# Kernel tuning notes

Measured on AMD Instinct MI355X. Metric: run time of the kernel, lower is better.

The kernel has to match this reference:

```python
import jax, jax.numpy as jnp
import numpy as np

B, TQ, TK = 4, 128, 512
DQ = DK = DV = H = 1024


def setup_inputs() -> dict:
    key = jax.random.key(0)
    ks = jax.random.split(key, 7)
    s = 0.05  # keep tanh out of saturation
    return {
        "query": jax.random.normal(ks[0], (B, TQ, DQ), dtype=jnp.float32),
        "key": jax.random.normal(ks[1], (B, TK, DK), dtype=jnp.float32),
        "value": jax.random.normal(ks[2], (B, TK, DV), dtype=jnp.float32),
        "Wq": jax.random.normal(ks[3], (DQ, H), dtype=jnp.float32) * s,
        "bq": jax.random.normal(ks[4], (H,), dtype=jnp.float32) * s,
        "Wk": jax.random.normal(ks[5], (DK, H), dtype=jnp.float32) * s,
        "v": jax.random.normal(ks[6], (H,), dtype=jnp.float32) * s,
    }


def reference(query, key, value, Wq, bq, Wk, v):
    # additive (Bahdanau) attention
    wq = jnp.einsum("bqd,dh->bqh", query, Wq) + bq      # [B,Tq,H]
    uh = jnp.einsum("bkd,dh->bkh", key, Wk)             # [B,Tk,H]
    # broadcast add -> [B,Tq,Tk,H], tanh, project to scalar score
    scores = jnp.einsum("bqkh,h->bqk",
                        jnp.tanh(wq[:, :, None, :] + uh[:, None, :, :]), v)
    attn = jax.nn.softmax(scores, axis=-1)              # [B,Tq,Tk]
    h = jnp.einsum("bqk,bkv->bqv", attn, value)         # [B,Tq,Dv]
    return h, attn
```

## Files before the change

### kernel.cpp

```cpp
#include <hip/hip_runtime.h>
#include <hip/hip_bf16.h>

typedef float f32x4 __attribute__((ext_vector_type(4)));
typedef float f32x2 __attribute__((ext_vector_type(2)));
typedef short s16x8 __attribute__((ext_vector_type(8)));
typedef short s16x4 __attribute__((ext_vector_type(4)));

#define NB  4
#define NTQ 128
#define NTK 512
#define NH  1024

__device__ __forceinline__ unsigned short f2bf(float x) {
    unsigned u = __builtin_bit_cast(unsigned, x);
    u += 0x7FFFu + ((u >> 16) & 1u);
    return (unsigned short)(u >> 16);
}

#define K2E  2.8853900817779268f

#define GLD16(gp, lp) __builtin_amdgcn_global_load_lds( \
    (const __attribute__((address_space(1))) unsigned int*)(gp), \
    (__attribute__((address_space(3))) unsigned int*)(lp), 16, 0, 0)

__global__ __launch_bounds__(256) void prep_kernel(
    const float* __restrict__ Q, const float* __restrict__ K,
    const float* __restrict__ Wq, const float* __restrict__ Wk,
    const float* __restrict__ value,
    short* __restrict__ Qb, short* __restrict__ Kb,
    short* __restrict__ WqT, short* __restrict__ WkT, short* __restrict__ valT)
{
    const int t = threadIdx.x, bx = blockIdx.x;
    if (bx < 640) {
        const float* src; short* dst; size_t base;
        if (bx < 128) { src = Q; dst = Qb; base = (size_t)bx * 4096; }
        else          { src = K; dst = Kb; base = (size_t)(bx - 128) * 4096; }
        #pragma unroll
        for (int i = 0; i < 4; ++i) {
            const size_t off = base + (size_t)(i * 256 + t) * 4;
            const float4 vv = *(const float4*)(src + off);
            s16x4 o = { (short)f2bf(vv.x), (short)f2bf(vv.y),
                        (short)f2bf(vv.z), (short)f2bf(vv.w) };
            *(s16x4*)(dst + off) = o;
        }
        return;
    }
    __shared__ float tile[64][65];
    const int i = bx - 640;
    const float* src; short* dst; int Cs, Rs, r0, c0;
    if (i < 256)      { src = Wq; dst = WqT; Cs = 1024; Rs = 1024; r0 = (i >> 4) * 64; c0 = (i & 15) * 64; }
    else if (i < 512) { const int j = i - 256; src = Wk; dst = WkT; Cs = 1024; Rs = 1024; r0 = (j >> 4) * 64; c0 = (j & 15) * 64; }
    else {
        const int j = i - 512, b = j >> 7, ti = j & 127;
        src = value + (size_t)b * 512 * 1024; dst = valT + (size_t)b * 1024 * 512;
        Cs = 1024; Rs = 512; r0 = (ti >> 4) * 64; c0 = (ti & 15) * 64;
    }
    {
        const int c = (t & 15) * 4;
        #pragma unroll
        for (int it = 0; it < 4; ++it) {
            const int r = (t >> 4) + it * 16;
            const float4 vv = *(const float4*)(src + (size_t)(r0 + r) * Cs + c0 + c);
            tile[r][c + 0] = vv.x; tile[r][c + 1] = vv.y;
            tile[r][c + 2] = vv.z; tile[r][c + 3] = vv.w;
        }
    }
    __syncthreads();
    {
        const int r = (t & 15) * 4;
        #pragma unroll
        for (int it = 0; it < 4; ++it) {
            const int c = (t >> 4) + it * 16;
            s16x4 o = { (short)f2bf(tile[r + 0][c]), (short)f2bf(tile[r + 1][c]),
                        (short)f2bf(tile[r + 2][c]), (short)f2bf(tile[r + 3][c]) };
            *(s16x4*)(dst + (size_t)(c0 + c) * Rs + r0 + r) = o;
        }
    }
}

__global__ __launch_bounds__(256) void mm_kernel(
    const short* __restrict__ Qb, const short* __restrict__ Kb,
    const short* __restrict__ WqT, const short* __restrict__ WkT,
    const float* __restrict__ bq,
    float* __restrict__ Ea_out, unsigned short* __restrict__ EbT)
{
    __shared__ short ldsA[2][128][64];
    __shared__ short ldsB[2][64][64];
    const int t = threadIdx.x;
    const int bx0 = blockIdx.x;
    const int bx = (bx0 & 7) * 40 + (bx0 >> 3);
    const bool g1 = bx < 64;
    const short *A, *B; int m0, n0;
    if (g1) { A = Qb; B = WqT; m0 = (bx >> 4) * 128; n0 = (bx & 15) * 64; }
    else    { const int i = bx - 64; A = Kb; B = WkT; m0 = (i >> 4) * 128; n0 = (i & 15) * 64; }
    A += (size_t)m0 * 1024; B += (size_t)n0 * 1024;

    f32x4 acc[4][2];
    #pragma unroll
    for (int i = 0; i < 4; ++i)
        #pragma unroll
        for (int j = 0; j < 2; ++j) acc[i][j] = f32x4{0.f, 0.f, 0.f, 0.f};

    const int lane = t & 63, wid = t >> 6;
    const int wr = wid >> 1, wc = wid & 1;
    const int fr = lane & 15, fko = (lane >> 4) * 16;

    #define STAGE_MM(buf, k0) do {                                              \
        _Pragma("unroll")                                                       \
        for (int it = 0; it < 4; ++it) {                                        \
            const int idx = it * 256 + t;                                       \
            const int row = idx >> 3, c16 = idx & 7;                            \
            const int sc = c16 ^ (row & 7);                                     \
            GLD16(A + (size_t)row * 1024 + (k0) + sc * 8,                       \
                  &ldsA[buf][0][0] + idx * 8);                                  \
        }                                                                       \
        _Pragma("unroll")                                                       \
        for (int it = 0; it < 2; ++it) {                                        \
            const int idx = it * 256 + t;                                       \
            const int row = idx >> 3, c16 = idx & 7;                            \
            const int sc = c16 ^ (row & 7);                                     \
            GLD16(B + (size_t)row * 1024 + (k0) + sc * 8,                       \
                  &ldsB[buf][0][0] + idx * 8);                                  \
        }                                                                       \
    } while (0)

    #define COMPUTE_MM(buf) do {                                                \
        _Pragma("unroll")                                                       \
        for (int kk = 0; kk < 2; ++kk) {                                        \
            s16x8 af[4], bfv[2];                                                \
            _Pragma("unroll")                                                   \
            for (int i = 0; i < 4; ++i) {                                       \
                const int rowA = wr * 64 + i * 16 + fr;                         \
                int offA = rowA * 128 + kk * 64 + fko; offA ^= (rowA & 7) << 4; \
                af[i] = *(const s16x8*)((const char*)&ldsA[buf][0][0] + offA);  \
            }                                                                   \
            _Pragma("unroll")                                                   \
            for (int ni = 0; ni < 2; ++ni) {                                    \
                const int rowB = wc * 32 + ni * 16 + fr;                        \
                int offB = rowB * 128 + kk * 64 + fko; offB ^= (rowB & 7) << 4; \
                bfv[ni] = *(const s16x8*)((const char*)&ldsB[buf][0][0] + offB);\
            }                                                                   \
            _Pragma("unroll")                                                   \
            for (int mi = 0; mi < 4; ++mi)                                      \
                _Pragma("unroll")                                               \
                for (int ni = 0; ni < 2; ++ni)                                  \
                    acc[mi][ni] = __builtin_amdgcn_mfma_f32_16x16x32_bf16(      \
                                      af[mi], bfv[ni], acc[mi][ni], 0, 0, 0);   \
        }                                                                       \
    } while (0)

    STAGE_MM(0, 0);
    __syncthreads();
    int cur = 0;
    for (int s = 0; s < 15; ++s) {
        STAGE_MM(cur ^ 1, (s + 1) * 64);
        COMPUTE_MM(cur);
        __syncthreads();
        cur ^= 1;
    }
    COMPUTE_MM(cur);

    const int row0 = (lane >> 4) * 4;
    if (g1) {
        #pragma unroll
        for (int ni = 0; ni < 2; ++ni) {
            const int n = n0 + wc * 32 + ni * 16 + fr;
            const float bias = bq[n];
            #pragma unroll
            for (int mi = 0; mi < 4; ++mi) {
                const int m = m0 + wr * 64 + mi * 16 + row0;
                #pragma unroll
                for (int j = 0; j < 4; ++j)
                    Ea_out[(size_t)(m + j) * 1024 + n] =
                        __builtin_amdgcn_exp2f(K2E * (acc[mi][ni][j] + bias));
            }
        }
    } else {
        #pragma unroll
        for (int mi = 0; mi < 4; ++mi) {
            const int m = m0 + wr * 64 + mi * 16 + row0;
            const int b = m >> 9, kk = m & 511;
            #pragma unroll
            for (int ni = 0; ni < 2; ++ni) {
                const int n = n0 + wc * 32 + ni * 16 + fr;
                s16x4 ev;
                #pragma unroll
                for (int j = 0; j < 4; ++j)
                    ev[j] = (short)f2bf(__builtin_amdgcn_exp2f(K2E * acc[mi][ni][j]));
                *(s16x4*)&EbT[((size_t)b * 1024 + n) * 512 + kk] = ev;
            }
        }
    }
    #undef STAGE_MM
    #undef COMPUTE_MM
}

__global__ __launch_bounds__(1024, 8) void scores_softmax(
    const unsigned short* __restrict__ EbT, const float* __restrict__ Ea,
    const float* __restrict__ v,
    float* __restrict__ attn_out, short* __restrict__ attnb)
{
    __shared__ float4 s_eav[1024];
    __shared__ float  s_part[4][2][512];
    __shared__ float  s_red[16];
    const int t = threadIdx.x, bx = blockIdx.x;
    const int b = bx >> 6, q2 = bx & 63;
    const int bq0 = b * 128 + q2 * 2;
    const int kp = t & 255;
    const int hq = t >> 8;
    const int lane = t & 63, wid = t >> 6;

    s_eav[t] = make_float4(Ea[(size_t)(bq0 + 0) * 1024 + t],
                           Ea[(size_t)(bq0 + 1) * 1024 + t],
                           v[t], 0.f);
    __syncthreads();

    const int h0 = hq * 256;
    const unsigned* up = (const unsigned*)(EbT + ((size_t)b * 1024 + h0) * 512) + kp;
    f32x2 a0 = {0.f, 0.f};
    f32x2 a1 = {0.f, 0.f};
    #pragma unroll 8
    for (int h = 0; h < 256; ++h) {
        const unsigned ebb = up[(size_t)h * 256];
        const float eb0 = __builtin_bit_cast(float, ebb << 16);
        const float eb1 = __builtin_bit_cast(float, ebb & 0xFFFF0000u);
        const float4 e = s_eav[h0 + h];
        f32x2 p0 = f32x2{eb0, eb1} * e.x + 1.0f;
        f32x2 p1 = f32x2{eb0, eb1} * e.y + 1.0f;
        f32x2 r0 = {__builtin_amdgcn_rcpf(p0.x), __builtin_amdgcn_rcpf(p0.y)};
        f32x2 r1 = {__builtin_amdgcn_rcpf(p1.x), __builtin_amdgcn_rcpf(p1.y)};
        a0 += r0 * e.z;
        a1 += r1 * e.z;
    }
    *(f32x2*)&s_part[hq][0][kp * 2] = a0;
    *(f32x2*)&s_part[hq][1][kp * 2] = a1;
    __syncthreads();

    const int kk = t & 511, qq = t >> 9;
    const float z = -2.0f * (s_part[0][qq][kk] + s_part[1][qq][kk]
                           + s_part[2][qq][kk] + s_part[3][qq][kk]);

    float m = z;
    #pragma unroll
    for (int off = 32; off > 0; off >>= 1)
        m = fmaxf(m, __shfl_xor(m, off, 64));
    if (lane == 0) s_red[wid] = m;
    __syncthreads();
    float mx = s_red[qq * 8];
    #pragma unroll
    for (int w = 1; w < 8; ++w) mx = fmaxf(mx, s_red[qq * 8 + w]);
    const float p = __expf(z - mx);
    __syncthreads();

    float sl = p;
    #pragma unroll
    for (int off = 32; off > 0; off >>= 1)
        sl += __shfl_xor(sl, off, 64);
    if (lane == 0) s_red[wid] = sl;
    __syncthreads();
    float s = 0.f;
    #pragma unroll
    for (int w = 0; w < 8; ++w) s += s_red[qq * 8 + w];

    const float a = p * (1.0f / s);
    attn_out[(size_t)(bq0 + qq) * 512 + kk] = a;
    attnb[(size_t)(bq0 + qq) * 512 + kk] = (short)f2bf(a);
}

__global__ __launch_bounds__(256) void pv_gemm(
    const short* __restrict__ attnb, const short* __restrict__ valT,
    float* __restrict__ outh)
{
    __shared__ short ldsA[2][128][64];
    __shared__ short ldsB[2][64][64];
    const int t = threadIdx.x, bx = blockIdx.x;
    const int b = bx >> 4, nt = bx & 15;
    const int n0 = nt * 64;
    const short* A = attnb + (size_t)b * 128 * 512;
    const short* B = valT + (size_t)b * 1024 * 512 + (size_t)n0 * 512;

    f32x4 acc[4][2];
    #pragma unroll
    for (int i = 0; i < 4; ++i)
        #pragma unroll
        for (int j = 0; j < 2; ++j) acc[i][j] = f32x4{0.f, 0.f, 0.f, 0.f};

    const int lane = t & 63, wid = t >> 6;
    const int wr = wid >> 1, wc = wid & 1;
    const int fr = lane & 15, fko = (lane >> 4) * 16;

    #define STAGE_PV(buf, k0) do {                                              \
        _Pragma("unroll")                                                       \
        for (int it = 0; it < 4; ++it) {                                        \
            const int idx = it * 256 + t;                                       \
            const int row = idx >> 3, c16 = idx & 7;                            \
            const int sc = c16 ^ (row & 7);                                     \
            GLD16(A + (size_t)row * 512 + (k0) + sc * 8,                        \
                  &ldsA[buf][0][0] + idx * 8);                                  \
        }                                                                       \
        _Pragma("unroll")                                                       \
        for (int it = 0; it < 2; ++it) {                                        \
            const int idx = it * 256 + t;                                       \
            const int row = idx >> 3, c16 = idx & 7;                            \
            const int sc = c16 ^ (row & 7);                                     \
            GLD16(B + (size_t)row * 512 + (k0) + sc * 8,                        \
                  &ldsB[buf][0][0] + idx * 8);                                  \
        }                                                                       \
    } while (0)

    #define COMPUTE_PV(buf) do {                                                \
        _Pragma("unroll")                                                       \
        for (int kk = 0; kk < 2; ++kk) {                                        \
            s16x8 af[4], bfv[2];                                                \
            _Pragma("unroll")                                                   \
            for (int i = 0; i < 4; ++i) {                                       \
                const int rowA = wr * 64 + i * 16 + fr;                         \
                int offA = rowA * 128 + kk * 64 + fko; offA ^= (rowA & 7) << 4; \
                af[i] = *(const s16x8*)((const char*)&ldsA[buf][0][0] + offA);  \
            }                                                                   \
            _Pragma("unroll")                                                   \
            for (int ni = 0; ni < 2; ++ni) {                                    \
                const int rowB = wc * 32 + ni * 16 + fr;                        \
                int offB = rowB * 128 + kk * 64 + fko; offB ^= (rowB & 7) << 4; \
                bfv[ni] = *(const s16x8*)((const char*)&ldsB[buf][0][0] + offB);\
            }                                                                   \
            _Pragma("unroll")                                                   \
            for (int mi = 0; mi < 4; ++mi)                                      \
                _Pragma("unroll")                                               \
                for (int ni = 0; ni < 2; ++ni)                                  \
                    acc[mi][ni] = __builtin_amdgcn_mfma_f32_16x16x32_bf16(      \
                                      af[mi], bfv[ni], acc[mi][ni], 0, 0, 0);   \
        }                                                                       \
    } while (0)

    STAGE_PV(0, 0);
    __syncthreads();
    int cur = 0;
    for (int s = 0; s < 7; ++s) {
        STAGE_PV(cur ^ 1, (s + 1) * 64);
        COMPUTE_PV(cur);
        __syncthreads();
        cur ^= 1;
    }
    COMPUTE_PV(cur);

    const int row0 = (lane >> 4) * 4;
    #pragma unroll
    for (int ni = 0; ni < 2; ++ni) {
        const int n = n0 + wc * 32 + ni * 16 + fr;
        #pragma unroll
        for (int mi = 0; mi < 4; ++mi) {
            const int m = wr * 64 + mi * 16 + row0;
            #pragma unroll
            for (int j = 0; j < 4; ++j)
                outh[(size_t)(b * 128 + m + j) * 1024 + n] = acc[mi][ni][j];
        }
    }
    #undef STAGE_PV
    #undef COMPUTE_PV
}

extern "C" void kernel_launch(void* const* d_in, const int* in_sizes, int n_in,
                              void* d_out, int out_size, void* d_ws, size_t ws_size,
                              hipStream_t stream)
{
    const float* query = (const float*)d_in[0];
    const float* key   = (const float*)d_in[1];
    const float* value = (const float*)d_in[2];
    const float* Wq    = (const float*)d_in[3];
    const float* bq    = (const float*)d_in[4];
    const float* Wk    = (const float*)d_in[5];
    const float* v     = (const float*)d_in[6];
    float* out = (float*)d_out;

    char* w = (char*)d_ws;
    float*          ws_Ea  = (float*)w;
    unsigned short* ws_EbT = (unsigned short*)(w + (2u << 20));
    short* Qb     = (short*)(w + (6u << 20));
    short* Kb     = (short*)(w + (7u << 20));
    short* WqT    = (short*)(w + (11u << 20));
    short* WkT    = (short*)(w + (13u << 20));
    short* valT   = (short*)(w + (15u << 20));
    short* attnb  = (short*)(w + (19u << 20));

    float* out_h    = out;
    float* out_attn = out + (size_t)NB * NTQ * NH;

    prep_kernel   <<<dim3(1664), dim3(256),  0, stream>>>(query, key, Wq, Wk, value,
                                                          Qb, Kb, WqT, WkT, valT);
    mm_kernel     <<<dim3(320),  dim3(256),  0, stream>>>(Qb, Kb, WqT, WkT, bq, ws_Ea, ws_EbT);
    scores_softmax<<<dim3(256),  dim3(1024), 0, stream>>>(ws_EbT, ws_Ea, v, out_attn, attnb);
    pv_gemm       <<<dim3(64),   dim3(256),  0, stream>>>(attnb, valT, out_h);
}
```

Before: 73.29 us.

## Split scores kernel over key halves and move softmax to separate kernel

The fused scores+softmax kernel is split in two. A scores kernel runs 512 blocks, each covering half the key range over 2 queries, and writes raw scores to a workspace buffer. A separate 512-thread softmax kernel then normalizes each row. This doubles the parallelism of the dominant tanh/score stage, which had only 256 blocks for 256 CUs, at the cost of an extra launch and a round trip of the score matrix through global memory.

```diff
diff --git a/kernel.cpp b/kernel.cpp
--- a/kernel.cpp
+++ b/kernel.cpp
@@ -195,32 +195,32 @@
     #undef COMPUTE_MM
 }
 
-__global__ __launch_bounds__(1024, 8) void scores_softmax(
+__global__ __launch_bounds__(1024, 8) void scores_z(
     const unsigned short* __restrict__ EbT, const float* __restrict__ Ea,
-    const float* __restrict__ v,
-    float* __restrict__ attn_out, short* __restrict__ attnb)
+    const float* __restrict__ v, float* __restrict__ zout)
 {
     __shared__ float4 s_eav[1024];
-    __shared__ float  s_part[4][2][512];
-    __shared__ float  s_red[16];
+    __shared__ float  s_part[8][2][256];
     const int t = threadIdx.x, bx = blockIdx.x;
-    const int b = bx >> 6, q2 = bx & 63;
+    const int kh = bx & 1;
+    const int bq2 = bx >> 1;
+    const int b = bq2 >> 6, q2 = bq2 & 63;
     const int bq0 = b * 128 + q2 * 2;
-    const int kp = t & 255;
-    const int hq = t >> 8;
-    const int lane = t & 63, wid = t >> 6;
+    const int kp = t & 127;
+    const int hq = t >> 7;
 
     s_eav[t] = make_float4(Ea[(size_t)(bq0 + 0) * 1024 + t],
                            Ea[(size_t)(bq0 + 1) * 1024 + t],
                            v[t], 0.f);
     __syncthreads();
 
-    const int h0 = hq * 256;
-    const unsigned* up = (const unsigned*)(EbT + ((size_t)b * 1024 + h0) * 512) + kp;
+    const int h0 = hq * 128;
+    const unsigned* up = (const unsigned*)(EbT + ((size_t)b * 1024 + h0) * 512)
+                         + kh * 128 + kp;
     f32x2 a0 = {0.f, 0.f};
     f32x2 a1 = {0.f, 0.f};
     #pragma unroll 8
-    for (int h = 0; h < 256; ++h) {
+    for (int h = 0; h < 128; ++h) {
         const unsigned ebb = up[(size_t)h * 256];
         const float eb0 = __builtin_bit_cast(float, ebb << 16);
         const float eb1 = __builtin_bit_cast(float, ebb & 0xFFFF0000u);
@@ -236,9 +236,23 @@
     *(f32x2*)&s_part[hq][1][kp * 2] = a1;
     __syncthreads();
 
-    const int kk = t & 511, qq = t >> 9;
-    const float z = -2.0f * (s_part[0][qq][kk] + s_part[1][qq][kk]
-                           + s_part[2][qq][kk] + s_part[3][qq][kk]);
+    if (t < 512) {
+        const int kk = t & 255, qq = t >> 8;
+        float z = 0.f;
+        #pragma unroll
+        for (int j = 0; j < 8; ++j) z += s_part[j][qq][kk];
+        zout[(size_t)(bq0 + qq) * 512 + kh * 256 + kk] = -2.0f * z;
+    }
+}
+
+__global__ __launch_bounds__(512) void softmax_kernel(
+    const float* __restrict__ zin, float* __restrict__ attn_out,
+    short* __restrict__ attnb)
+{
+    __shared__ float s_red[16];
+    const int t = threadIdx.x, bqi = blockIdx.x;
+    const float z = zin[(size_t)bqi * 512 + t];
+    const int lane = t & 63, wid = t >> 6;
 
     float m = z;
     #pragma unroll
@@ -246,9 +260,9 @@
         m = fmaxf(m, __shfl_xor(m, off, 64));
     if (lane == 0) s_red[wid] = m;
     __syncthreads();
-    float mx = s_red[qq * 8];
-    #pragma unroll
-    for (int w = 1; w < 8; ++w) mx = fmaxf(mx, s_red[qq * 8 + w]);
+    float mx = s_red[0];
+    #pragma unroll
+    for (int w = 1; w < 8; ++w) mx = fmaxf(mx, s_red[w]);
     const float p = __expf(z - mx);
     __syncthreads();
 
@@ -260,11 +274,11 @@
     __syncthreads();
     float s = 0.f;
     #pragma unroll
-    for (int w = 0; w < 8; ++w) s += s_red[qq * 8 + w];
+    for (int w = 0; w < 8; ++w) s += s_red[w];
 
     const float a = p * (1.0f / s);
-    attn_out[(size_t)(bq0 + qq) * 512 + kk] = a;
-    attnb[(size_t)(bq0 + qq) * 512 + kk] = (short)f2bf(a);
+    attn_out[(size_t)bqi * 512 + t] = a;
+    attnb[(size_t)bqi * 512 + t] = (short)f2bf(a);
 }
 
 __global__ __launch_bounds__(256) void pv_gemm(
@@ -382,6 +396,7 @@
     short* WkT    = (short*)(w + (13u << 20));
     short* valT   = (short*)(w + (15u << 20));
     short* attnb  = (short*)(w + (19u << 20));
+    float* zbuf   = (float*)(w + (20u << 20));
 
     float* out_h    = out;
     float* out_attn = out + (size_t)NB * NTQ * NH;
@@ -389,6 +404,7 @@
     prep_kernel   <<<dim3(1664), dim3(256),  0, stream>>>(query, key, Wq, Wk, value,
                                                           Qb, Kb, WqT, WkT, valT);
     mm_kernel     <<<dim3(320),  dim3(256),  0, stream>>>(Qb, Kb, WqT, WkT, bq, ws_Ea, ws_EbT);
-    scores_softmax<<<dim3(256),  dim3(1024), 0, stream>>>(ws_EbT, ws_Ea, v, out_attn, attnb);
+    scores_z      <<<dim3(512),  dim3(1024), 0, stream>>>(ws_EbT, ws_Ea, v, zbuf);
+    softmax_kernel<<<dim3(512),  dim3(512),  0, stream>>>(zbuf, out_attn, attnb);
     pv_gemm       <<<dim3(64),   dim3(256),  0, stream>>>(attnb, valT, out_h);
 }
```

Result: no change. 72.66 us (-0.9%).
